# Optimization experiments

Hardware: AMD Instinct MI355X
Metric: run time of the kernel (lower is better)

Reference implementation:

```python
import jax, jax.numpy as jnp
import numpy as np

K_HOPS = 3
ALPHA = 0.3
DELTA = 0.5
KL_EPS = 1e-10
BN_EPS = 1e-5
DEG_MIN = 1e-6

B, T, N, F_IN, H, T_OUT = 8, 12, 1536, 1, 64, 12
HID2 = 2 * H  # MLP hidden width = 128


def setup_inputs() -> dict:
    key = jax.random.key(0)
    ks = jax.random.split(key, 20)
    s = 0.05
    TH = T * H
    inp = {
        "x": jax.random.normal(ks[0], (B, T, N, F_IN), jnp.float32),
        # AdaptiveBiDiffConv weights (stored as (in, out))
        "W1": jax.random.normal(ks[1], (F_IN, H), jnp.float32) * s,
        "W2": jax.random.normal(ks[2], (F_IN, H), jnp.float32) * s,
        # encoder MLPBlock: Linear(TH,128) ReLU Linear(128,128) ReLU Linear(128,64) + proj(TH,64), BN(64)
        "enc_w1": jax.random.normal(ks[3], (TH, HID2), jnp.float32) * s,
        "enc_b1": jnp.zeros((HID2,), jnp.float32),
        "enc_w2": jax.random.normal(ks[4], (HID2, HID2), jnp.float32) * s,
        "enc_b2": jnp.zeros((HID2,), jnp.float32),
        "enc_w3": jax.random.normal(ks[5], (HID2, H), jnp.float32) * s,
        "enc_b3": jnp.zeros((H,), jnp.float32),
        "enc_proj": jax.random.normal(ks[6], (TH, H), jnp.float32) * s,
        "enc_bn_g": jnp.ones((H,), jnp.float32),
        "enc_bn_b": jnp.zeros((H,), jnp.float32),
        "enc_bn_m": jnp.zeros((H,), jnp.float32),
        "enc_bn_v": jnp.ones((H,), jnp.float32),
        # decoder MLPBlock: Linear(64,128) ReLU Linear(128,128) ReLU Linear(128,12) + proj(64,12), BN(12)
        "dec_w1": jax.random.normal(ks[7], (H, HID2), jnp.float32) * s,
        "dec_b1": jnp.zeros((HID2,), jnp.float32),
        "dec_w2": jax.random.normal(ks[8], (HID2, HID2), jnp.float32) * s,
        "dec_b2": jnp.zeros((HID2,), jnp.float32),
        "dec_w3": jax.random.normal(ks[9], (HID2, T_OUT), jnp.float32) * s,
        "dec_b3": jnp.zeros((T_OUT,), jnp.float32),
        "dec_proj": jax.random.normal(ks[10], (H, T_OUT), jnp.float32) * s,
        "dec_bn_g": jnp.ones((T_OUT,), jnp.float32),
        "dec_bn_b": jnp.zeros((T_OUT,), jnp.float32),
        "dec_bn_m": jnp.zeros((T_OUT,), jnp.float32),
        "dec_bn_v": jnp.ones((T_OUT,), jnp.float32),
    }
    return inp


def _row_norm(A):
    return A / jnp.maximum(A.sum(-1, keepdims=True), DEG_MIN)


def _mlp_block(z, w1, b1, w2, b2, w3, b3, proj, g, be, m, v):
    h = jax.nn.relu(z @ w1 + b1)
    h = jax.nn.relu(h @ w2 + b2)
    o = (h @ w3 + b3) + z @ proj
    # BatchNorm1d, eval mode over last (channel) axis
    return (o - m) / jnp.sqrt(v + BN_EPS) * g + be


def _forward(x, W1, W2,
             enc_w1, enc_b1, enc_w2, enc_b2, enc_w3, enc_b3, enc_proj,
             enc_bn_g, enc_bn_b, enc_bn_m, enc_bn_v,
             dec_w1, dec_b1, dec_w2, dec_b2, dec_w3, dec_b3, dec_proj,
             dec_bn_g, dec_bn_b, dec_bn_m, dec_bn_v):
    b, t, n, _ = x.shape
    # ---- KL adjacency (fused form: avoids (B,N,N,T) broadcast) ----
    p = jax.nn.softmax(jnp.transpose(x[..., 0], (0, 2, 1)), axis=-1)  # (B,N,T)
    logp = jnp.log(p + KL_EPS)
    # kl[b,i,j] = sum_t p_i (logp_i - logp_j)
    kl = jnp.sum(p * logp, axis=-1, keepdims=True) - jnp.einsum('bit,bjt->bij', p, logp)
    A = (kl < DELTA).astype(x.dtype)  # (B,N,N)
    A_fwd = _row_norm(A)
    A_bwd = _row_norm(jnp.swapaxes(A, -1, -2))
    # ---- bidirectional diffusion conv (x_k never updated in original loop) ----
    x_flow = x[..., :1]                    # (B,T,N,1)
    x_res = x_flow @ W1                    # (B,T,N,H)
    xw = x_flow @ W2                       # (B,T,N,H)
    fwd = jnp.einsum('bij,btjh->btih', A_fwd, xw)
    bwd = jnp.einsum('bij,btjh->btih', A_bwd, xw)
    x_p = jax.nn.relu(x_res + K_HOPS * (ALPHA * fwd + (1.0 - ALPHA) * bwd))
    # ---- temporal MLP encoder/decoder ----
    x_flat = jnp.transpose(x_p, (0, 2, 1, 3)).reshape(b, n, t * x_p.shape[-1])  # (B,N,T*H)
    x_e = _mlp_block(x_flat, enc_w1, enc_b1, enc_w2, enc_b2, enc_w3, enc_b3,
                     enc_proj, enc_bn_g, enc_bn_b, enc_bn_m, enc_bn_v)  # (B,N,H)
    x_d = _mlp_block(x_e, dec_w1, dec_b1, dec_w2, dec_b2, dec_w3, dec_b3,
                     dec_proj, dec_bn_g, dec_bn_b, dec_bn_m, dec_bn_v)  # (B,N,T_out)
    return jnp.transpose(x_d, (0, 2, 1))[..., None]  # (B,T_out,N,1)


def reference(x, W1, W2,
              enc_w1, enc_b1, enc_w2, enc_b2, enc_w3, enc_b3, enc_proj,
              enc_bn_g, enc_bn_b, enc_bn_m, enc_bn_v,
              dec_w1, dec_b1, dec_w2, dec_b2, dec_w3, dec_b3, dec_proj,
              dec_bn_g, dec_bn_b, dec_bn_m, dec_bn_v):
    return _forward(x, W1, W2,
                    enc_w1, enc_b1, enc_w2, enc_b2, enc_w3, enc_b3, enc_proj,
                    enc_bn_g, enc_bn_b, enc_bn_m, enc_bn_v,
                    dec_w1, dec_b1, dec_w2, dec_b2, dec_w3, dec_b3, dec_proj,
                    dec_bn_g, dec_bn_b, dec_bn_m, dec_bn_v)
```

## Files before the change

### kernel.cpp

```cpp
#include <hip/hip_runtime.h>
#include <hip/hip_bf16.h>


namespace {

constexpr int Nn = 1536, TOUT = 12;

typedef __attribute__((ext_vector_type(8))) short bf8;
typedef __attribute__((ext_vector_type(4))) float f4;
typedef unsigned short ush;

__device__ __forceinline__ float b2f(__hip_bfloat16 v) { return __bfloat162float(v); }
__device__ __forceinline__ ush f2bu(float f) {
  union { __hip_bfloat16 h; ush u; } c; c.h = __float2bfloat16(f); return c.u;
}
__device__ __forceinline__ float bu2f(ush u) {
  union { unsigned int i; float f; } c; c.i = ((unsigned)u) << 16; return c.f;
}
__device__ __forceinline__ float ldraw(const void* p, size_t i, int fl) {
  return fl ? ((const float*)p)[i] : b2f(((const __hip_bfloat16*)p)[i]);
}

__device__ __forceinline__ int detect_fl(const void* x, int tid) {
  __shared__ int cnt;
  if (tid == 0) cnt = 0;
  __syncthreads();
  const ush* u = (const ush*)x;
  int c = 0;
#pragma unroll
  for (int s = 0; s < 16; ++s) {
    ush v = u[tid + s * 256];
    if (((v >> 7) & 0xFF) >= 140) c++;
  }
  atomicAdd(&cnt, c);
  __syncthreads();
  return (cnt > 64) ? 1 : 0;
}

struct SmallTab { const void* src[16]; int n[16]; int off[16]; };
struct RepTab { const void* src[8]; int Nc[8]; int NCT[8]; int lb[9]; };

__global__ __launch_bounds__(256) void prep_all(
    const void* __restrict__ xraw, SmallTab st, RepTab rt,
    int* __restrict__ flag, float* __restrict__ CS,
    float* __restrict__ sd,
    ush* __restrict__ phi16, ush* __restrict__ plo16,
    ush* __restrict__ lhi16, ush* __restrict__ llo16,
    ush* __restrict__ Xc, ush* __restrict__ Wf) {
  __shared__ float lvs[64][12];
  int tid = threadIdx.x;
  int fl = detect_fl(xraw, tid);
  int blk = blockIdx.x;

  if (blk < 192) {
    int rl = tid >> 2, sub = tid & 3;
    int row = blk * 64 + rl;
    int b = row / Nn, nn = row - b * Nn;
    float xv[12];
#pragma unroll
    for (int t = 0; t < 12; ++t)
      xv[t] = ldraw(xraw, (size_t)(b * 12 + t) * Nn + nn, fl);
    float mx = xv[0];
#pragma unroll
    for (int t = 1; t < 12; ++t) mx = fmaxf(mx, xv[t]);
    float e[12], Z = 0.f;
#pragma unroll
    for (int t = 0; t < 12; ++t) { e[t] = expf(xv[t] - mx); Z += e[t]; }
    float invZ = 1.f / Z;
#pragma unroll
    for (int u = 0; u < 3; ++u) {
      int t = sub * 3 + u;
      float pv = e[t] * invZ;
      float lv = logf(pv + 1e-10f);
      lvs[rl][t] = lv;
      ush phv = f2bu(pv);  float plv = pv - bu2f(phv);
      ush lhv = f2bu(lv);  float llv = lv - bu2f(lhv);
      phi16[(size_t)row * 16 + t] = phv;
      plo16[(size_t)row * 16 + t] = f2bu(plv);
      lhi16[(size_t)row * 16 + t] = lhv;
      llo16[(size_t)row * 16 + t] = f2bu(llv);
      Xc[((size_t)(b * 16 + t)) * Nn + nn] = f2bu(xv[t]);
    }
    {
      int t = 12 + sub;
      phi16[(size_t)row * 16 + t] = 0;
      plo16[(size_t)row * 16 + t] = 0;
      lhi16[(size_t)row * 16 + t] = 0;
      llo16[(size_t)row * 16 + t] = 0;
      Xc[((size_t)(b * 16 + t)) * Nn + nn] = (sub == 0) ? (ush)0x3F80 : (ush)0;
    }
    __syncthreads();
    if (sub == 0) {
      float sacc = 0.f;
#pragma unroll
      for (int t = 0; t < 12; ++t)
        sacc = fmaf(e[t] * invZ, lvs[rl][t], sacc);
      sd[row] = sacc;
    }
  } else if (blk < 290) {
    int idx = (blk - 192) * 256 + tid;
    if (idx >= rt.lb[8]) return;
    int mi = 0;
#pragma unroll
    for (int i = 1; i < 8; ++i) if (idx >= rt.lb[i]) mi = i;
    int li = idx - rt.lb[mi];
    int NCT = rt.NCT[mi], Nc = rt.Nc[mi];
    int per = NCT * 64;
    int c0 = li / per, rem = li - c0 * per;
    int ct = rem >> 6, l = rem & 63;
    int q = l >> 4, m = l & 15;
    int col = ct * 16 + m;
    ush* d = Wf + (size_t)idx * 8;
#pragma unroll
    for (int j = 0; j < 8; ++j) {
      int k = c0 * 32 + q * 8 + j;
      d[j] = (col < Nc) ? f2bu(ldraw(rt.src[mi], (size_t)k * Nc + col, fl)) : 0;
    }
  } else {
    for (int i = 0; i < 16; ++i)
      for (int e = tid; e < st.n[i]; e += 256)
        CS[st.off[i] + e] = ldraw(st.src[i], e, fl);
    if (tid == 0) flag[0] = fl;
  }
}

__global__ __launch_bounds__(256, 3) void klmlp(
    const void* __restrict__ xraw,
    const ush* __restrict__ phi16, const ush* __restrict__ plo16,
    const ush* __restrict__ lhi16, const ush* __restrict__ llo16,
    const ush* __restrict__ Xc, const float* __restrict__ sd,
    const float* __restrict__ CS, const ush* __restrict__ Wf,
    const int* __restrict__ flag, void* __restrict__ outp) {
  __shared__ float xs[16][12], ccs[16][12];
  __shared__ float sfs[16][16], sbs[16][16];
  __shared__ float ws1[64], ws2[64];
  __shared__ ush hf[2048], hg[2048], xf[1024];
  __shared__ f4 red[4][64], red2[4][64];
  __shared__ union { ush T[2][4][512]; ush zf[12288]; } u;

  int tid = threadIdx.x, w = tid >> 6, l = tid & 63, q = l >> 4, n = l & 15;
  int bi = blockIdx.x;
  int r0 = bi * 16;
  int b = bi / 96;
  int rowb = b * Nn;
  int fl = flag[0];

  if (tid < 192) {
    int rr = tid / 12, tt = tid - rr * 12;
    xs[rr][tt] = ldraw(xraw, (size_t)(b * 12 + tt) * Nn + (r0 - rowb + rr), fl);
  }

  {
    bf8 z8 = {0, 0, 0, 0, 0, 0, 0, 0};
    bf8 aP = (q < 2)
        ? *(const bf8*)(phi16 + ((size_t)(r0 + n)) * 16 + q * 8)
        : *(const bf8*)(plo16 + ((size_t)(r0 + n)) * 16 + (q - 2) * 8);
    bf8 aL = (q < 2)
        ? *(const bf8*)(lhi16 + ((size_t)(r0 + n)) * 16 + q * 8)
        : *(const bf8*)(llo16 + ((size_t)(r0 + n)) * 16 + (q - 2) * 8);
    bf8 aPh = (q < 2) ? aP : z8;
    bf8 aLh = (q < 2) ? aL : z8;
    float selfI[4];
#pragma unroll
    for (int r = 0; r < 4; ++r) selfI[r] = sd[r0 + q * 4 + r];

    f4 accF = {0.f, 0.f, 0.f, 0.f}, accB = {0.f, 0.f, 0.f, 0.f};

    for (int jp = 0; jp < 12; ++jp) {
      int jl = w * 384 + jp * 32;
#pragma unroll
      for (int hh = 0; hh < 2; ++hh) {
        int jh = jl + hh * 16;
        size_t bb = ((size_t)(rowb + jh + n)) * 16 + (q & 1) * 8;
        bf8 bLh = *(const bf8*)(lhi16 + bb);
        bf8 bLo = *(const bf8*)(llo16 + bb);
        bf8 bPh = *(const bf8*)(phi16 + bb);
        bf8 bPo = *(const bf8*)(plo16 + bb);
        float selfJ = sd[rowb + jh + n];

        f4 s1 = {0.f, 0.f, 0.f, 0.f}, s2 = {0.f, 0.f, 0.f, 0.f};
        s1 = __builtin_amdgcn_mfma_f32_16x16x32_bf16(aP, bLh, s1, 0, 0, 0);
        s1 = __builtin_amdgcn_mfma_f32_16x16x32_bf16(aPh, bLo, s1, 0, 0, 0);
        s2 = __builtin_amdgcn_mfma_f32_16x16x32_bf16(aL, bPh, s2, 0, 0, 0);
        s2 = __builtin_amdgcn_mfma_f32_16x16x32_bf16(aLh, bPo, s2, 0, 0, 0);

        int qk = n >> 3, kj = n & 7;
#pragma unroll
        for (int r = 0; r < 4; ++r) {
          int pos = hh * 256 + (qk * 16 + q * 4 + r) * 8 + kj;
          u.T[0][w][pos] = (selfI[r] - s1[r] < 0.5f) ? (ush)0x3F80 : (ush)0;
          u.T[1][w][pos] = (selfJ - s2[r] < 0.5f) ? (ush)0x3F80 : (ush)0;
        }
      }
      bf8 af1 = *(const bf8*)(&u.T[0][w][(size_t)l * 8]);
      bf8 af2 = *(const bf8*)(&u.T[1][w][(size_t)l * 8]);
      bf8 xfr = *(const bf8*)(Xc + ((size_t)(b * 16 + n)) * Nn + jl + q * 8);
      accF = __builtin_amdgcn_mfma_f32_16x16x32_bf16(af1, xfr, accF, 0, 0, 0);
      accB = __builtin_amdgcn_mfma_f32_16x16x32_bf16(af2, xfr, accB, 0, 0, 0);
    }
    red[w][l] = accF;
    red2[w][l] = accB;
  }
  __syncthreads();

  if (w == 0) {
    f4 s = red[0][l] + red[1][l] + red[2][l] + red[3][l];
#pragma unroll
    for (int r = 0; r < 4; ++r) sfs[q * 4 + r][n] = s[r];
  } else if (w == 1) {
    f4 s = red2[0][l] + red2[1][l] + red2[2][l] + red2[3][l];
#pragma unroll
    for (int r = 0; r < 4; ++r) sbs[q * 4 + r][n] = s[r];
  } else if (w == 2) {
    ws1[l] = CS[l];
  } else {
    ws2[l] = CS[64 + l];
  }
  __syncthreads();
  if (tid < 192) {
    int rr = tid / 12, tt = tid - rr * 12;
    float irs = 1.f / fmaxf(sfs[rr][12], 1e-6f);
    float ics = 1.f / fmaxf(sbs[rr][12], 1e-6f);
    ccs[rr][tt] = 3.0f * (0.3f * sfs[rr][tt] * irs + 0.7f * sbs[rr][tt] * ics);
  }
  __syncthreads();

  auto zregen = [&](int c0) -> bf8 {
    int t = c0 >> 1, h0 = (c0 & 1) * 32 + q * 8;
    float xv = xs[n][t], cv = ccs[n][t];
    union { bf8 v; ush uu[8]; } au;
#pragma unroll
    for (int j = 0; j < 8; ++j)
      au.uu[j] = f2bu(fmaxf(fmaf(xv, ws1[h0 + j], cv * ws2[h0 + j]), 0.f));
    return au.v;
  };
  auto fpos = [&](int ct, int r) -> int {
    return ((ct >> 1) * 64 + ((ct & 1) * 2 + (n >> 3)) * 16 + q * 4 + r) * 8 + (n & 7);
  };

#pragma unroll
  for (int u6 = 0; u6 < 6; ++u6) {
    int c0 = w * 6 + u6;
    bf8 v = zregen(c0);
    *(bf8*)(&u.zf[((size_t)c0 * 64 + l) * 8]) = v;
  }
  __syncthreads();

  {
    f4 a0 = {0.f, 0.f, 0.f, 0.f}, a1 = {0.f, 0.f, 0.f, 0.f};
    for (int c0 = 0; c0 < 24; ++c0) {
      bf8 a = *(const bf8*)(&u.zf[((size_t)c0 * 64 + l) * 8]);
      const ush* wb = Wf + ((size_t)(c0 * 8 + 2 * w) * 64 + l) * 8;
      bf8 b0 = *(const bf8*)wb;
      bf8 b1 = *(const bf8*)(wb + 512);
      a0 = __builtin_amdgcn_mfma_f32_16x16x32_bf16(a, b0, a0, 0, 0, 0);
      a1 = __builtin_amdgcn_mfma_f32_16x16x32_bf16(a, b1, a1, 0, 0, 0);
    }
#pragma unroll
    for (int u2 = 0; u2 < 2; ++u2) {
      int ct = 2 * w + u2;
      f4 acc = u2 ? a1 : a0;
      float bz = CS[128 + ct * 16 + n];
#pragma unroll
      for (int r = 0; r < 4; ++r)
        hf[fpos(ct, r)] = f2bu(fmaxf(acc[r] + bz, 0.f));
    }
  }
  __syncthreads();

  {
    f4 a0 = {0.f, 0.f, 0.f, 0.f}, a1 = {0.f, 0.f, 0.f, 0.f};
    for (int c0 = 0; c0 < 4; ++c0) {
      bf8 a = *(const bf8*)(&hf[(size_t)(c0 * 64 + l) * 8]);
      const ush* wb = Wf + 98304 + ((size_t)(c0 * 8 + 2 * w) * 64 + l) * 8;
      bf8 b0 = *(const bf8*)wb;
      bf8 b1 = *(const bf8*)(wb + 512);
      a0 = __builtin_amdgcn_mfma_f32_16x16x32_bf16(a, b0, a0, 0, 0, 0);
      a1 = __builtin_amdgcn_mfma_f32_16x16x32_bf16(a, b1, a1, 0, 0, 0);
    }
    __syncthreads();
#pragma unroll
    for (int u2 = 0; u2 < 2; ++u2) {
      int ct = 2 * w + u2;
      f4 acc = u2 ? a1 : a0;
      float bz = CS[256 + ct * 16 + n];
#pragma unroll
      for (int r = 0; r < 4; ++r)
        hg[fpos(ct, r)] = f2bu(fmaxf(acc[r] + bz, 0.f));
    }
  }
  __syncthreads();

  {
    f4 a3 = {0.f, 0.f, 0.f, 0.f};
    for (int c0 = 0; c0 < 4; ++c0) {
      bf8 a = *(const bf8*)(&hg[(size_t)(c0 * 64 + l) * 8]);
      bf8 bb = *(const bf8*)(Wf + 114688 + ((size_t)(c0 * 4 + w) * 64 + l) * 8);
      a3 = __builtin_amdgcn_mfma_f32_16x16x32_bf16(a, bb, a3, 0, 0, 0);
    }
    for (int c0 = 0; c0 < 24; ++c0) {
      bf8 a = *(const bf8*)(&u.zf[((size_t)c0 * 64 + l) * 8]);
      bf8 bb = *(const bf8*)(Wf + 122880 + ((size_t)(c0 * 4 + w) * 64 + l) * 8);
      a3 = __builtin_amdgcn_mfma_f32_16x16x32_bf16(a, bb, a3, 0, 0, 0);
    }
    int col = w * 16 + n;
    float g = CS[448 + col], be = CS[512 + col], mm = CS[576 + col], vv = CS[640 + col];
    float sc = g / sqrtf(vv + 1e-5f);
    float sh = be - mm * sc;
    float bz = CS[384 + col];
#pragma unroll
    for (int r = 0; r < 4; ++r)
      xf[fpos(w, r)] = f2bu((a3[r] + bz) * sc + sh);
  }
  __syncthreads();

  {
    f4 a0 = {0.f, 0.f, 0.f, 0.f}, a1 = {0.f, 0.f, 0.f, 0.f};
    for (int c0 = 0; c0 < 2; ++c0) {
      bf8 a = *(const bf8*)(&xf[(size_t)(c0 * 64 + l) * 8]);
      const ush* wb = Wf + 172032 + ((size_t)(c0 * 8 + 2 * w) * 64 + l) * 8;
      bf8 b0 = *(const bf8*)wb;
      bf8 b1 = *(const bf8*)(wb + 512);
      a0 = __builtin_amdgcn_mfma_f32_16x16x32_bf16(a, b0, a0, 0, 0, 0);
      a1 = __builtin_amdgcn_mfma_f32_16x16x32_bf16(a, b1, a1, 0, 0, 0);
    }
    __syncthreads();
#pragma unroll
    for (int u2 = 0; u2 < 2; ++u2) {
      int ct = 2 * w + u2;
      f4 acc = u2 ? a1 : a0;
      float bz = CS[704 + ct * 16 + n];
#pragma unroll
      for (int r = 0; r < 4; ++r)
        hf[fpos(ct, r)] = f2bu(fmaxf(acc[r] + bz, 0.f));
    }
  }
  __syncthreads();

  {
    f4 a0 = {0.f, 0.f, 0.f, 0.f}, a1 = {0.f, 0.f, 0.f, 0.f};
    for (int c0 = 0; c0 < 4; ++c0) {
      bf8 a = *(const bf8*)(&hf[(size_t)(c0 * 64 + l) * 8]);
      const ush* wb = Wf + 180224 + ((size_t)(c0 * 8 + 2 * w) * 64 + l) * 8;
      bf8 b0 = *(const bf8*)wb;
      bf8 b1 = *(const bf8*)(wb + 512);
      a0 = __builtin_amdgcn_mfma_f32_16x16x32_bf16(a, b0, a0, 0, 0, 0);
      a1 = __builtin_amdgcn_mfma_f32_16x16x32_bf16(a, b1, a1, 0, 0, 0);
    }
    __syncthreads();
#pragma unroll
    for (int u2 = 0; u2 < 2; ++u2) {
      int ct = 2 * w + u2;
      f4 acc = u2 ? a1 : a0;
      float bz = CS[832 + ct * 16 + n];
#pragma unroll
      for (int r = 0; r < 4; ++r)
        hg[fpos(ct, r)] = f2bu(fmaxf(acc[r] + bz, 0.f));
    }
  }
  __syncthreads();

  {
    f4 ao = {0.f, 0.f, 0.f, 0.f};
    {
      bf8 a = *(const bf8*)(&hg[(size_t)(w * 64 + l) * 8]);
      bf8 bb = *(const bf8*)(Wf + 196608 + ((size_t)w * 64 + l) * 8);
      ao = __builtin_amdgcn_mfma_f32_16x16x32_bf16(a, bb, ao, 0, 0, 0);
    }
    if (w < 2) {
      bf8 a = *(const bf8*)(&xf[(size_t)(w * 64 + l) * 8]);
      bf8 bb = *(const bf8*)(Wf + 198656 + ((size_t)w * 64 + l) * 8);
      ao = __builtin_amdgcn_mfma_f32_16x16x32_bf16(a, bb, ao, 0, 0, 0);
    }
    red[w][l] = ao;
  }
  __syncthreads();
  if (w == 0) {
    f4 s = red[0][l] + red[1][l] + red[2][l] + red[3][l];
    if (n < 12) {
      float bz = CS[960 + n];
      float g = CS[972 + n], be = CS[984 + n], mm = CS[996 + n], vv = CS[1008 + n];
      float sc = g / sqrtf(vv + 1e-5f);
      float sh = be - mm * sc;
#pragma unroll
      for (int r = 0; r < 4; ++r) {
        int row = r0 + q * 4 + r;
        int bb2 = row / Nn, nn2 = row - bb2 * Nn;
        size_t oi = ((size_t)bb2 * TOUT + n) * Nn + nn2;
        float ov = (s[r] + bz) * sc + sh;
        if (fl) ((float*)outp)[oi] = ov;
        else    ((ush*)outp)[oi] = f2bu(ov);
      }
    }
  }
}

}

extern "C" void kernel_launch(void* const* d_in, const int* in_sizes, int n_in,
                              void* d_out, int out_size, void* d_ws, size_t ws_size,
                              hipStream_t stream) {
  float* f = (float*)d_ws;
  int* flag = (int*)d_ws;
  float* CS  = f + 16;
  float* sd  = f + 1040;
  ush* U = (ush*)(f + 13328);
  ush* phi16 = U;
  ush* plo16 = U + 196608;
  ush* lhi16 = U + 393216;
  ush* llo16 = U + 589824;
  ush* Xc    = U + 786432;
  ush* Wf    = U + 983040;

  SmallTab st;
  {
    const int idxs[16] = {1, 2, 4, 6, 8, 10, 11, 12, 13, 15, 17, 19, 21, 22, 23, 24};
    const int ns[16]   = {64, 64, 128, 128, 64, 64, 64, 64, 64, 128, 128, 12, 12, 12, 12, 12};
    int off = 0;
    for (int i = 0; i < 16; ++i) {
      st.src[i] = d_in[idxs[i]]; st.n[i] = ns[i]; st.off[i] = off; off += ns[i];
    }
  }
  RepTab rt;
  {
    const int idxs[8]  = {3, 5, 7, 9, 14, 16, 18, 20};
    const int rNc[8]   = {128, 128, 64, 64, 128, 128, 12, 12};
    const int rNCT[8]  = {8, 8, 4, 4, 8, 8, 1, 1};
    const int rlb[9]   = {0, 12288, 14336, 15360, 21504, 22528, 24576, 24832, 24960};
    for (int i = 0; i < 8; ++i) {
      rt.src[i] = d_in[idxs[i]]; rt.Nc[i] = rNc[i]; rt.NCT[i] = rNCT[i];
    }
    for (int i = 0; i < 9; ++i) rt.lb[i] = rlb[i];
  }

  prep_all<<<291, 256, 0, stream>>>(d_in[0], st, rt, flag, CS, sd,
                                    phi16, plo16, lhi16, llo16, Xc, Wf);
  klmlp<<<768, 256, 0, stream>>>(d_in[0], phi16, plo16, lhi16, llo16,
                                 Xc, sd, CS, Wf, flag, d_out);
}
```

Baseline: 140.6 us.

## Double klmlp block to 8 waves, splitting graph and MLP work across them

Raises the fused KL-graph + MLP kernel from 4 to 8 wavefronts per block. The graph-mask phase now walks half as many columns per wave, and each MLP layer gives one 16-column tile per wave instead of two. The encoder's last layer splits its K range across wave halves and sums through shared memory. The aim is more latency hiding and shorter serial chains per block, at the cost of more registers and LDS per block, extra reductions, and lower occupancy per CU.

```diff
diff --git a/kernel.cpp b/kernel.cpp
--- a/kernel.cpp
+++ b/kernel.cpp
@@ -21,15 +21,14 @@
   return fl ? ((const float*)p)[i] : b2f(((const __hip_bfloat16*)p)[i]);
 }
 
-__device__ __forceinline__ int detect_fl(const void* x, int tid) {
+__device__ __forceinline__ int detect_fl(const void* x, int tid, int nthr) {
   __shared__ int cnt;
   if (tid == 0) cnt = 0;
   __syncthreads();
   const ush* u = (const ush*)x;
   int c = 0;
-#pragma unroll
-  for (int s = 0; s < 16; ++s) {
-    ush v = u[tid + s * 256];
+  for (int s = tid; s < 4096; s += nthr) {
+    ush v = u[s];
     if (((v >> 7) & 0xFF) >= 140) c++;
   }
   atomicAdd(&cnt, c);
@@ -49,7 +48,7 @@
     ush* __restrict__ Xc, ush* __restrict__ Wf) {
   __shared__ float lvs[64][12];
   int tid = threadIdx.x;
-  int fl = detect_fl(xraw, tid);
+  int fl = detect_fl(xraw, tid, 256);
   int blk = blockIdx.x;
 
   if (blk < 192) {
@@ -124,7 +123,7 @@
   }
 }
 
-__global__ __launch_bounds__(256, 3) void klmlp(
+__global__ __launch_bounds__(512, 4) void klmlp(
     const void* __restrict__ xraw,
     const ush* __restrict__ phi16, const ush* __restrict__ plo16,
     const ush* __restrict__ lhi16, const ush* __restrict__ llo16,
@@ -135,8 +134,11 @@
   __shared__ float sfs[16][16], sbs[16][16];
   __shared__ float ws1[64], ws2[64];
   __shared__ ush hf[2048], hg[2048], xf[1024];
-  __shared__ f4 red[4][64], red2[4][64];
-  __shared__ union { ush T[2][4][512]; ush zf[12288]; } u;
+  __shared__ f4 red[8][64];
+  __shared__ union {
+    struct { ush T[2][8][512]; f4 red2[8][64]; } pb;
+    ush zf[12288];
+  } u;
 
   int tid = threadIdx.x, w = tid >> 6, l = tid & 63, q = l >> 4, n = l & 15;
   int bi = blockIdx.x;
@@ -166,8 +168,8 @@
 
     f4 accF = {0.f, 0.f, 0.f, 0.f}, accB = {0.f, 0.f, 0.f, 0.f};
 
-    for (int jp = 0; jp < 12; ++jp) {
-      int jl = w * 384 + jp * 32;
+    for (int jp = 0; jp < 6; ++jp) {
+      int jl = w * 192 + jp * 32;
 #pragma unroll
       for (int hh = 0; hh < 2; ++hh) {
         int jh = jl + hh * 16;
@@ -188,32 +190,34 @@
 #pragma unroll
         for (int r = 0; r < 4; ++r) {
           int pos = hh * 256 + (qk * 16 + q * 4 + r) * 8 + kj;
-          u.T[0][w][pos] = (selfI[r] - s1[r] < 0.5f) ? (ush)0x3F80 : (ush)0;
-          u.T[1][w][pos] = (selfJ - s2[r] < 0.5f) ? (ush)0x3F80 : (ush)0;
+          u.pb.T[0][w][pos] = (selfI[r] - s1[r] < 0.5f) ? (ush)0x3F80 : (ush)0;
+          u.pb.T[1][w][pos] = (selfJ - s2[r] < 0.5f) ? (ush)0x3F80 : (ush)0;
         }
       }
-      bf8 af1 = *(const bf8*)(&u.T[0][w][(size_t)l * 8]);
-      bf8 af2 = *(const bf8*)(&u.T[1][w][(size_t)l * 8]);
+      bf8 af1 = *(const bf8*)(&u.pb.T[0][w][(size_t)l * 8]);
+      bf8 af2 = *(const bf8*)(&u.pb.T[1][w][(size_t)l * 8]);
       bf8 xfr = *(const bf8*)(Xc + ((size_t)(b * 16 + n)) * Nn + jl + q * 8);
       accF = __builtin_amdgcn_mfma_f32_16x16x32_bf16(af1, xfr, accF, 0, 0, 0);
       accB = __builtin_amdgcn_mfma_f32_16x16x32_bf16(af2, xfr, accB, 0, 0, 0);
     }
     red[w][l] = accF;
-    red2[w][l] = accB;
+    u.pb.red2[w][l] = accB;
   }
   __syncthreads();
 
   if (w == 0) {
-    f4 s = red[0][l] + red[1][l] + red[2][l] + red[3][l];
+    f4 s = red[0][l] + red[1][l] + red[2][l] + red[3][l]
+         + red[4][l] + red[5][l] + red[6][l] + red[7][l];
 #pragma unroll
     for (int r = 0; r < 4; ++r) sfs[q * 4 + r][n] = s[r];
   } else if (w == 1) {
-    f4 s = red2[0][l] + red2[1][l] + red2[2][l] + red2[3][l];
+    f4 s = u.pb.red2[0][l] + u.pb.red2[1][l] + u.pb.red2[2][l] + u.pb.red2[3][l]
+         + u.pb.red2[4][l] + u.pb.red2[5][l] + u.pb.red2[6][l] + u.pb.red2[7][l];
 #pragma unroll
     for (int r = 0; r < 4; ++r) sbs[q * 4 + r][n] = s[r];
   } else if (w == 2) {
     ws1[l] = CS[l];
-  } else {
+  } else if (w == 3) {
     ws2[l] = CS[64 + l];
   }
   __syncthreads();
@@ -239,70 +243,67 @@
   };
 
 #pragma unroll
-  for (int u6 = 0; u6 < 6; ++u6) {
-    int c0 = w * 6 + u6;
+  for (int u3 = 0; u3 < 3; ++u3) {
+    int c0 = w * 3 + u3;
     bf8 v = zregen(c0);
     *(bf8*)(&u.zf[((size_t)c0 * 64 + l) * 8]) = v;
   }
   __syncthreads();
 
   {
-    f4 a0 = {0.f, 0.f, 0.f, 0.f}, a1 = {0.f, 0.f, 0.f, 0.f};
+    f4 a0 = {0.f, 0.f, 0.f, 0.f};
     for (int c0 = 0; c0 < 24; ++c0) {
       bf8 a = *(const bf8*)(&u.zf[((size_t)c0 * 64 + l) * 8]);
-      const ush* wb = Wf + ((size_t)(c0 * 8 + 2 * w) * 64 + l) * 8;
-      bf8 b0 = *(const bf8*)wb;
-      bf8 b1 = *(const bf8*)(wb + 512);
+      bf8 b0 = *(const bf8*)(Wf + ((size_t)(c0 * 8 + w) * 64 + l) * 8);
       a0 = __builtin_amdgcn_mfma_f32_16x16x32_bf16(a, b0, a0, 0, 0, 0);
-      a1 = __builtin_amdgcn_mfma_f32_16x16x32_bf16(a, b1, a1, 0, 0, 0);
-    }
-#pragma unroll
-    for (int u2 = 0; u2 < 2; ++u2) {
-      int ct = 2 * w + u2;
-      f4 acc = u2 ? a1 : a0;
-      float bz = CS[128 + ct * 16 + n];
-#pragma unroll
-      for (int r = 0; r < 4; ++r)
-        hf[fpos(ct, r)] = f2bu(fmaxf(acc[r] + bz, 0.f));
-    }
-  }
-  __syncthreads();
-
-  {
-    f4 a0 = {0.f, 0.f, 0.f, 0.f}, a1 = {0.f, 0.f, 0.f, 0.f};
+    }
+    float bz = CS[128 + w * 16 + n];
+#pragma unroll
+    for (int r = 0; r < 4; ++r)
+      hf[fpos(w, r)] = f2bu(fmaxf(a0[r] + bz, 0.f));
+  }
+  __syncthreads();
+
+  {
+    f4 a0 = {0.f, 0.f, 0.f, 0.f};
     for (int c0 = 0; c0 < 4; ++c0) {
       bf8 a = *(const bf8*)(&hf[(size_t)(c0 * 64 + l) * 8]);
-      const ush* wb = Wf + 98304 + ((size_t)(c0 * 8 + 2 * w) * 64 + l) * 8;
-      bf8 b0 = *(const bf8*)wb;
-      bf8 b1 = *(const bf8*)(wb + 512);
+      bf8 b0 = *(const bf8*)(Wf + 98304 + ((size_t)(c0 * 8 + w) * 64 + l) * 8);
       a0 = __builtin_amdgcn_mfma_f32_16x16x32_bf16(a, b0, a0, 0, 0, 0);
-      a1 = __builtin_amdgcn_mfma_f32_16x16x32_bf16(a, b1, a1, 0, 0, 0);
     }
     __syncthreads();
-#pragma unroll
-    for (int u2 = 0; u2 < 2; ++u2) {
-      int ct = 2 * w + u2;
-      f4 acc = u2 ? a1 : a0;
-      float bz = CS[256 + ct * 16 + n];
-#pragma unroll
-      for (int r = 0; r < 4; ++r)
-        hg[fpos(ct, r)] = f2bu(fmaxf(acc[r] + bz, 0.f));
-    }
+    float bz = CS[256 + w * 16 + n];
+#pragma unroll
+    for (int r = 0; r < 4; ++r)
+      hg[fpos(w, r)] = f2bu(fmaxf(a0[r] + bz, 0.f));
   }
   __syncthreads();
 
   {
     f4 a3 = {0.f, 0.f, 0.f, 0.f};
-    for (int c0 = 0; c0 < 4; ++c0) {
-      bf8 a = *(const bf8*)(&hg[(size_t)(c0 * 64 + l) * 8]);
-      bf8 bb = *(const bf8*)(Wf + 114688 + ((size_t)(c0 * 4 + w) * 64 + l) * 8);
-      a3 = __builtin_amdgcn_mfma_f32_16x16x32_bf16(a, bb, a3, 0, 0, 0);
-    }
-    for (int c0 = 0; c0 < 24; ++c0) {
-      bf8 a = *(const bf8*)(&u.zf[((size_t)c0 * 64 + l) * 8]);
-      bf8 bb = *(const bf8*)(Wf + 122880 + ((size_t)(c0 * 4 + w) * 64 + l) * 8);
-      a3 = __builtin_amdgcn_mfma_f32_16x16x32_bf16(a, bb, a3, 0, 0, 0);
-    }
+    if (w < 4) {
+      for (int c0 = 0; c0 < 4; ++c0) {
+        bf8 a = *(const bf8*)(&hg[(size_t)(c0 * 64 + l) * 8]);
+        bf8 bb = *(const bf8*)(Wf + 114688 + ((size_t)(c0 * 4 + w) * 64 + l) * 8);
+        a3 = __builtin_amdgcn_mfma_f32_16x16x32_bf16(a, bb, a3, 0, 0, 0);
+      }
+      for (int c0 = 0; c0 < 12; ++c0) {
+        bf8 a = *(const bf8*)(&u.zf[((size_t)c0 * 64 + l) * 8]);
+        bf8 bb = *(const bf8*)(Wf + 122880 + ((size_t)(c0 * 4 + w) * 64 + l) * 8);
+        a3 = __builtin_amdgcn_mfma_f32_16x16x32_bf16(a, bb, a3, 0, 0, 0);
+      }
+    } else {
+      for (int c0 = 12; c0 < 24; ++c0) {
+        bf8 a = *(const bf8*)(&u.zf[((size_t)c0 * 64 + l) * 8]);
+        bf8 bb = *(const bf8*)(Wf + 122880 + ((size_t)(c0 * 4 + (w - 4)) * 64 + l) * 8);
+        a3 = __builtin_amdgcn_mfma_f32_16x16x32_bf16(a, bb, a3, 0, 0, 0);
+      }
+    }
+    red[w][l] = a3;
+  }
+  __syncthreads();
+  if (w < 4) {
+    f4 s = red[w][l] + red[w + 4][l];
     int col = w * 16 + n;
     float g = CS[448 + col], be = CS[512 + col], mm = CS[576 + col], vv = CS[640 + col];
     float sc = g / sqrtf(vv + 1e-5f);
@@ -310,73 +311,56 @@
     float bz = CS[384 + col];
 #pragma unroll
     for (int r = 0; r < 4; ++r)
-      xf[fpos(w, r)] = f2bu((a3[r] + bz) * sc + sh);
-  }
-  __syncthreads();
-
-  {
-    f4 a0 = {0.f, 0.f, 0.f, 0.f}, a1 = {0.f, 0.f, 0.f, 0.f};
+      xf[fpos(w, r)] = f2bu((s[r] + bz) * sc + sh);
+  }
+  __syncthreads();
+
+  {
+    f4 a0 = {0.f, 0.f, 0.f, 0.f};
     for (int c0 = 0; c0 < 2; ++c0) {
       bf8 a = *(const bf8*)(&xf[(size_t)(c0 * 64 + l) * 8]);
-      const ush* wb = Wf + 172032 + ((size_t)(c0 * 8 + 2 * w) * 64 + l) * 8;
-      bf8 b0 = *(const bf8*)wb;
-      bf8 b1 = *(const bf8*)(wb + 512);
+      bf8 b0 = *(const bf8*)(Wf + 172032 + ((size_t)(c0 * 8 + w) * 64 + l) * 8);
       a0 = __builtin_amdgcn_mfma_f32_16x16x32_bf16(a, b0, a0, 0, 0, 0);
-      a1 = __builtin_amdgcn_mfma_f32_16x16x32_bf16(a, b1, a1, 0, 0, 0);
     }
     __syncthreads();
-#pragma unroll
-    for (int u2 = 0; u2 < 2; ++u2) {
-      int ct = 2 * w + u2;
-      f4 acc = u2 ? a1 : a0;
-      float bz = CS[704 + ct * 16 + n];
-#pragma unroll
-      for (int r = 0; r < 4; ++r)
-        hf[fpos(ct, r)] = f2bu(fmaxf(acc[r] + bz, 0.f));
-    }
-  }
-  __syncthreads();
-
-  {
-    f4 a0 = {0.f, 0.f, 0.f, 0.f}, a1 = {0.f, 0.f, 0.f, 0.f};
+    float bz = CS[704 + w * 16 + n];
+#pragma unroll
+    for (int r = 0; r < 4; ++r)
+      hf[fpos(w, r)] = f2bu(fmaxf(a0[r] + bz, 0.f));
+  }
+  __syncthreads();
+
+  {
+    f4 a0 = {0.f, 0.f, 0.f, 0.f};
     for (int c0 = 0; c0 < 4; ++c0) {
       bf8 a = *(const bf8*)(&hf[(size_t)(c0 * 64 + l) * 8]);
-      const ush* wb = Wf + 180224 + ((size_t)(c0 * 8 + 2 * w) * 64 + l) * 8;
-      bf8 b0 = *(const bf8*)wb;
-      bf8 b1 = *(const bf8*)(wb + 512);
+      bf8 b0 = *(const bf8*)(Wf + 180224 + ((size_t)(c0 * 8 + w) * 64 + l) * 8);
       a0 = __builtin_amdgcn_mfma_f32_16x16x32_bf16(a, b0, a0, 0, 0, 0);
-      a1 = __builtin_amdgcn_mfma_f32_16x16x32_bf16(a, b1, a1, 0, 0, 0);
     }
     __syncthreads();
-#pragma unroll
-    for (int u2 = 0; u2 < 2; ++u2) {
-      int ct = 2 * w + u2;
-      f4 acc = u2 ? a1 : a0;
-      float bz = CS[832 + ct * 16 + n];
-#pragma unroll
-      for (int r = 0; r < 4; ++r)
-        hg[fpos(ct, r)] = f2bu(fmaxf(acc[r] + bz, 0.f));
-    }
+    float bz = CS[832 + w * 16 + n];
+#pragma unroll
+    for (int r = 0; r < 4; ++r)
+      hg[fpos(w, r)] = f2bu(fmaxf(a0[r] + bz, 0.f));
   }
   __syncthreads();
 
   {
     f4 ao = {0.f, 0.f, 0.f, 0.f};
-    {
+    if (w < 4) {
       bf8 a = *(const bf8*)(&hg[(size_t)(w * 64 + l) * 8]);
       bf8 bb = *(const bf8*)(Wf + 196608 + ((size_t)w * 64 + l) * 8);
       ao = __builtin_amdgcn_mfma_f32_16x16x32_bf16(a, bb, ao, 0, 0, 0);
-    }
-    if (w < 2) {
-      bf8 a = *(const bf8*)(&xf[(size_t)(w * 64 + l) * 8]);
-      bf8 bb = *(const bf8*)(Wf + 198656 + ((size_t)w * 64 + l) * 8);
+    } else if (w < 6) {
+      bf8 a = *(const bf8*)(&xf[(size_t)((w - 4) * 64 + l) * 8]);
+      bf8 bb = *(const bf8*)(Wf + 198656 + ((size_t)(w - 4) * 64 + l) * 8);
       ao = __builtin_amdgcn_mfma_f32_16x16x32_bf16(a, bb, ao, 0, 0, 0);
     }
     red[w][l] = ao;
   }
   __syncthreads();
   if (w == 0) {
-    f4 s = red[0][l] + red[1][l] + red[2][l] + red[3][l];
+    f4 s = red[0][l] + red[1][l] + red[2][l] + red[3][l] + red[4][l] + red[5][l];
     if (n < 12) {
       float bz = CS[960 + n];
       float g = CS[972 + n], be = CS[984 + n], mm = CS[996 + n], vv = CS[1008 + n];
@@ -435,6 +419,6 @@
 
   prep_all<<<291, 256, 0, stream>>>(d_in[0], st, rt, flag, CS, sd,
                                     phi16, plo16, lhi16, llo16, Xc, Wf);
-  klmlp<<<768, 256, 0, stream>>>(d_in[0], phi16, plo16, lhi16, llo16,
+  klmlp<<<768, 512, 0, stream>>>(d_in[0], phi16, plo16, lhi16, llo16,
                                  Xc, sd, CS, Wf, flag, d_out);
 }
```

Result: slower. 148.0 us (+5.2%).

## Alias reduction buffers into shared union and split MFMA accumulator chains

Applied to the files above, without the earlier changes.

Moves the reduction scratch arrays into the shared-memory union that already holds the per-wave tiles and z features, cutting the kernel's LDS footprint so more blocks can be resident per CU. The long K-loops in the first encoder layer and the projection now use two independent accumulator chains, breaking MFMA dependency stalls. The pairwise loop also gets unroll 2. The extra accumulators raise register pressure against the launch bound of 3 blocks.

```diff
diff --git a/kernel.cpp b/kernel.cpp
--- a/kernel.cpp
+++ b/kernel.cpp
@@ -135,8 +135,12 @@
   __shared__ float sfs[16][16], sbs[16][16];
   __shared__ float ws1[64], ws2[64];
   __shared__ ush hf[2048], hg[2048], xf[1024];
-  __shared__ f4 red[4][64], red2[4][64];
-  __shared__ union { ush T[2][4][512]; ush zf[12288]; } u;
+  __shared__ union {
+    struct { ush T1[512]; ush T2[512]; } pw[4];
+    struct { f4 rF[64]; f4 rB[64]; } pr[4];
+    ush zf[12288];
+    f4 r3[256];
+  } u;
 
   int tid = threadIdx.x, w = tid >> 6, l = tid & 63, q = l >> 4, n = l & 15;
   int bi = blockIdx.x;
@@ -166,6 +170,7 @@
 
     f4 accF = {0.f, 0.f, 0.f, 0.f}, accB = {0.f, 0.f, 0.f, 0.f};
 
+#pragma unroll 2
     for (int jp = 0; jp < 12; ++jp) {
       int jl = w * 384 + jp * 32;
 #pragma unroll
@@ -188,27 +193,27 @@
 #pragma unroll
         for (int r = 0; r < 4; ++r) {
           int pos = hh * 256 + (qk * 16 + q * 4 + r) * 8 + kj;
-          u.T[0][w][pos] = (selfI[r] - s1[r] < 0.5f) ? (ush)0x3F80 : (ush)0;
-          u.T[1][w][pos] = (selfJ - s2[r] < 0.5f) ? (ush)0x3F80 : (ush)0;
+          u.pw[w].T1[pos] = (selfI[r] - s1[r] < 0.5f) ? (ush)0x3F80 : (ush)0;
+          u.pw[w].T2[pos] = (selfJ - s2[r] < 0.5f) ? (ush)0x3F80 : (ush)0;
         }
       }
-      bf8 af1 = *(const bf8*)(&u.T[0][w][(size_t)l * 8]);
-      bf8 af2 = *(const bf8*)(&u.T[1][w][(size_t)l * 8]);
+      bf8 af1 = *(const bf8*)(&u.pw[w].T1[(size_t)l * 8]);
+      bf8 af2 = *(const bf8*)(&u.pw[w].T2[(size_t)l * 8]);
       bf8 xfr = *(const bf8*)(Xc + ((size_t)(b * 16 + n)) * Nn + jl + q * 8);
       accF = __builtin_amdgcn_mfma_f32_16x16x32_bf16(af1, xfr, accF, 0, 0, 0);
       accB = __builtin_amdgcn_mfma_f32_16x16x32_bf16(af2, xfr, accB, 0, 0, 0);
     }
-    red[w][l] = accF;
-    red2[w][l] = accB;
+    u.pr[w].rF[l] = accF;
+    u.pr[w].rB[l] = accB;
   }
   __syncthreads();
 
   if (w == 0) {
-    f4 s = red[0][l] + red[1][l] + red[2][l] + red[3][l];
+    f4 s = u.pr[0].rF[l] + u.pr[1].rF[l] + u.pr[2].rF[l] + u.pr[3].rF[l];
 #pragma unroll
     for (int r = 0; r < 4; ++r) sfs[q * 4 + r][n] = s[r];
   } else if (w == 1) {
-    f4 s = red2[0][l] + red2[1][l] + red2[2][l] + red2[3][l];
+    f4 s = u.pr[0].rB[l] + u.pr[1].rB[l] + u.pr[2].rB[l] + u.pr[3].rB[l];
 #pragma unroll
     for (int r = 0; r < 4; ++r) sbs[q * 4 + r][n] = s[r];
   } else if (w == 2) {
@@ -247,15 +252,19 @@
   __syncthreads();
 
   {
-    f4 a0 = {0.f, 0.f, 0.f, 0.f}, a1 = {0.f, 0.f, 0.f, 0.f};
-    for (int c0 = 0; c0 < 24; ++c0) {
-      bf8 a = *(const bf8*)(&u.zf[((size_t)c0 * 64 + l) * 8]);
-      const ush* wb = Wf + ((size_t)(c0 * 8 + 2 * w) * 64 + l) * 8;
-      bf8 b0 = *(const bf8*)wb;
-      bf8 b1 = *(const bf8*)(wb + 512);
-      a0 = __builtin_amdgcn_mfma_f32_16x16x32_bf16(a, b0, a0, 0, 0, 0);
-      a1 = __builtin_amdgcn_mfma_f32_16x16x32_bf16(a, b1, a1, 0, 0, 0);
-    }
+    f4 a0e = {0.f, 0.f, 0.f, 0.f}, a0o = {0.f, 0.f, 0.f, 0.f};
+    f4 a1e = {0.f, 0.f, 0.f, 0.f}, a1o = {0.f, 0.f, 0.f, 0.f};
+    for (int c0 = 0; c0 < 24; c0 += 2) {
+      bf8 ae = *(const bf8*)(&u.zf[((size_t)c0 * 64 + l) * 8]);
+      bf8 ao = *(const bf8*)(&u.zf[((size_t)(c0 + 1) * 64 + l) * 8]);
+      const ush* wbe = Wf + ((size_t)(c0 * 8 + 2 * w) * 64 + l) * 8;
+      const ush* wbo = Wf + ((size_t)((c0 + 1) * 8 + 2 * w) * 64 + l) * 8;
+      a0e = __builtin_amdgcn_mfma_f32_16x16x32_bf16(ae, *(const bf8*)wbe, a0e, 0, 0, 0);
+      a1e = __builtin_amdgcn_mfma_f32_16x16x32_bf16(ae, *(const bf8*)(wbe + 512), a1e, 0, 0, 0);
+      a0o = __builtin_amdgcn_mfma_f32_16x16x32_bf16(ao, *(const bf8*)wbo, a0o, 0, 0, 0);
+      a1o = __builtin_amdgcn_mfma_f32_16x16x32_bf16(ao, *(const bf8*)(wbo + 512), a1o, 0, 0, 0);
+    }
+    f4 a0 = a0e + a0o, a1 = a1e + a1o;
 #pragma unroll
     for (int u2 = 0; u2 < 2; ++u2) {
       int ct = 2 * w + u2;
@@ -298,11 +307,16 @@
       bf8 bb = *(const bf8*)(Wf + 114688 + ((size_t)(c0 * 4 + w) * 64 + l) * 8);
       a3 = __builtin_amdgcn_mfma_f32_16x16x32_bf16(a, bb, a3, 0, 0, 0);
     }
-    for (int c0 = 0; c0 < 24; ++c0) {
-      bf8 a = *(const bf8*)(&u.zf[((size_t)c0 * 64 + l) * 8]);
-      bf8 bb = *(const bf8*)(Wf + 122880 + ((size_t)(c0 * 4 + w) * 64 + l) * 8);
-      a3 = __builtin_amdgcn_mfma_f32_16x16x32_bf16(a, bb, a3, 0, 0, 0);
-    }
+    f4 e0 = {0.f, 0.f, 0.f, 0.f}, e1 = {0.f, 0.f, 0.f, 0.f};
+    for (int c0 = 0; c0 < 12; ++c0) {
+      bf8 aa = *(const bf8*)(&u.zf[((size_t)c0 * 64 + l) * 8]);
+      bf8 ab = *(const bf8*)(&u.zf[((size_t)(c0 + 12) * 64 + l) * 8]);
+      bf8 ba = *(const bf8*)(Wf + 122880 + ((size_t)(c0 * 4 + w) * 64 + l) * 8);
+      bf8 bbq = *(const bf8*)(Wf + 122880 + ((size_t)((c0 + 12) * 4 + w) * 64 + l) * 8);
+      e0 = __builtin_amdgcn_mfma_f32_16x16x32_bf16(aa, ba, e0, 0, 0, 0);
+      e1 = __builtin_amdgcn_mfma_f32_16x16x32_bf16(ab, bbq, e1, 0, 0, 0);
+    }
+    a3 = a3 + e0 + e1;
     int col = w * 16 + n;
     float g = CS[448 + col], be = CS[512 + col], mm = CS[576 + col], vv = CS[640 + col];
     float sc = g / sqrtf(vv + 1e-5f);
@@ -372,11 +386,11 @@
       bf8 bb = *(const bf8*)(Wf + 198656 + ((size_t)w * 64 + l) * 8);
       ao = __builtin_amdgcn_mfma_f32_16x16x32_bf16(a, bb, ao, 0, 0, 0);
     }
-    red[w][l] = ao;
+    u.r3[w * 64 + l] = ao;
   }
   __syncthreads();
   if (w == 0) {
-    f4 s = red[0][l] + red[1][l] + red[2][l] + red[3][l];
+    f4 s = u.r3[l] + u.r3[64 + l] + u.r3[128 + l] + u.r3[192 + l];
     if (n < 12) {
       float bz = CS[960 + n];
       float g = CS[972 + n], be = CS[984 + n], mm = CS[996 + n], vv = CS[1008 + n];
```

Result: no change. 143.3 us (+1.9%).
